# Optimization experiments

Hardware: AMD Instinct MI355X
Metric: run time of the kernel (lower is better)

The kernel has to match this reference:

```python
import itertools
import jax, jax.numpy as jnp
import numpy as np

THR = 0.2  # success_threshold (non-trainable constant)
V = 2      # num_total_variables
U_IDX, B_IDX = 1, 2  # rule_idxs for arities [0,1,2]


def _perm_indices(num_objects: int, v: int):
    """Static permutation index tables (numpy, shapes are compile-time)."""
    perm_idxs = np.array(list(itertools.permutations(range(num_objects), v)))  # [P, V]
    bidx = np.stack(np.nonzero(1 - np.eye(v))).T.reshape(v, v - 1, 2)          # [V, V-1, 2]
    pb = perm_idxs[:, bidx]                                                     # [P, V, V-1, 2]
    shift = (pb[..., 1] > pb[..., 0]).astype(np.int64)
    perm_bidxs = np.stack([pb[..., 0], pb[..., 1] - shift], axis=-1)            # off-diagonal compact idx
    return jnp.asarray(perm_idxs), jnp.asarray(perm_bidxs)


def setup_inputs() -> dict:
    key = jax.random.key(0)
    k1, k2, k3, k4, k5 = jax.random.split(key, 5)
    B, O, P0, P1, P2, C = 16, 64, 128, 128, 128, 8
    num_in = P0 + V * P1 + V * (V - 1) * P2  # 640
    return {
        "nullary": jax.random.normal(k1, (B, P0), dtype=jnp.float32),
        "unary": jax.random.normal(k2, (B, O, P1), dtype=jnp.float32),
        "binary": jax.random.normal(k3, (B, O, O - 1, P2), dtype=jnp.float32),
        "and_kernel": 0.01 * jax.random.normal(k4, (3, C, num_in), dtype=jnp.float32),
        "or_kernel": 0.01 * jax.random.normal(k5, (3, C), dtype=jnp.float32),
    }


def _forward(nullary, unary, binary, and_kernel, or_kernel):
    B, O, _ = unary.shape
    perm_idxs, perm_bidxs = _perm_indices(O, V)
    P = perm_idxs.shape[0]  # O*(O-1) for V=2
    thr = jnp.float32(THR)

    # permutation gathers -> flatten_concat with batch_dims=2
    pn = jnp.broadcast_to(nullary[:, None], (B, P, nullary.shape[-1]))          # [B,P,P0]
    pu = unary[:, perm_idxs].reshape(B, P, -1)                                   # [B,P,V*P1]
    pb = binary[:, perm_bidxs[..., 0], perm_bidxs[..., 1]].reshape(B, P, -1)     # [B,P,V*(V-1)*P2]
    x = jnp.concatenate([pn, pu, pb], axis=-1)                                   # [B,P,num_in]

    # AND stage: multiply-sum + bias + tanh (einsum == sum(in_tensor * and_kernel, -1))
    and_bias = thr - jnp.sum(jnp.square(and_kernel), -1) * jnp.tanh(thr)         # [A,C]
    conj = jnp.tanh(jnp.einsum('bpi,aci->bpac', x, and_kernel) + and_bias)       # [B,P,A,C]

    A, C = and_kernel.shape[0], and_kernel.shape[1]
    # OR max-reduce over unused permutation dims
    null_r = jnp.max(conj[:, :, :U_IDX, :], axis=1)                              # [B,n0,C]
    un_r = conj[:, :, U_IDX:B_IDX, :].reshape(B, O, P // O, B_IDX - U_IDX, C).max(axis=2)
    bi_r = conj[:, :, B_IDX:, :].reshape(B, O, O - 1, P // (O * (O - 1)), A - B_IDX, C).max(axis=3)

    def or_stage(c, k):
        bias = jnp.sum(jnp.square(k), -1) * jnp.tanh(thr) - thr                  # [n_rules]
        return jnp.einsum('...rc,rc->...r', c, k) + bias

    return (or_stage(null_r, or_kernel[:U_IDX]),
            or_stage(un_r, or_kernel[U_IDX:B_IDX]),
            or_stage(bi_r, or_kernel[B_IDX:]))


def reference(nullary, unary, binary, and_kernel, or_kernel):
    # outputs: nullary [B,1], unary [B,O,1], binary [B,O,O-1,1]
    return _forward(nullary, unary, binary, and_kernel, or_kernel)
```

## Files before the change

kernel.cpp:

```cpp
#include <hip/hip_runtime.h>

#define THR_F     0.2f
#define TANH_THR  0.19737532f

__device__ __forceinline__ float fast_tanh(float x) {
    x = fminf(10.f, fmaxf(-10.f, x));
    float e = __expf(2.f * x);
    return (e - 1.f) * __builtin_amdgcn_rcpf(e + 1.f);
}

__device__ __forceinline__ unsigned fkey(float f) {
    unsigned u = __float_as_uint(f);
    return (u & 0x80000000u) ? ~u : (u | 0x80000000u);
}
__device__ __forceinline__ float fdecode(unsigned u) {
    return __uint_as_float((u & 0x80000000u) ? (u & 0x7FFFFFFFu) : ~u);
}

__global__ __launch_bounds__(64) void prep_kernel(
    const float* __restrict__ nullary,
    const float* __restrict__ andk,
    float* __restrict__ Wb,
    float* __restrict__ Wu,
    float* __restrict__ base,
    unsigned* __restrict__ max0)
{
    const int bid = blockIdx.x;
    const int t   = threadIdx.x;
    if (bid < 384) {
        const int b = bid / 24, n = bid % 24;
        const float* w  = andk + n * 640;
        const float* nu = nullary + b * 128;
        float s = 0.f;
        #pragma unroll
        for (int i = 0; i < 10; ++i) { float v = w[t + i * 64]; s = fmaf(v, v, s); }
        float d = fmaf(nu[t], w[t], 0.f);
        d = fmaf(nu[t + 64], w[t + 64], d);
        #pragma unroll
        for (int m = 32; m; m >>= 1) {
            s += __shfl_xor(s, m, 64);
            d += __shfl_xor(d, m, 64);
        }
        if (t == 0) base[bid] = d + THR_F - s * TANH_THR;
    } else {
        const int i = (bid - 384) * 64 + t;
        const int k = i / 48, n = i % 48;
        const int ac   = (n < 24) ? n : n - 24;
        const int colb = (n < 24) ? 384 : 512;
        const int colu = (n < 24) ? 128 : 256;
        Wb[i] = andk[ac * 640 + colb + k];
        Wu[i] = andk[ac * 640 + colu + k];
        if (bid < 386) max0[(bid - 384) * 64 + t] = 0u;
    }
}

__global__ __launch_bounds__(256) void proj_kernel(
    const float* __restrict__ unary,
    const float* __restrict__ binary,
    const float* __restrict__ Wb,
    const float* __restrict__ Wu,
    float* __restrict__ P0,
    float* __restrict__ P1T,
    float* __restrict__ U0, float* __restrict__ U1)
{
    const int bid  = blockIdx.x;
    const int wave = __builtin_amdgcn_readfirstlane((int)(threadIdx.x >> 6));
    const int lane = threadIdx.x & 63;
    const bool is_bin = (bid < 1008);

    const int row = is_bin ? (bid * 64 + lane) : ((bid - 1008) * 64 + lane);
    const float* __restrict__ W   = (is_bin ? Wb : Wu) + wave * 12;
    const float* __restrict__ src = (is_bin ? binary : unary) + (size_t)row * 128;

    float* dst;
    if (is_bin) {
        if (wave < 2) {
            dst = P0 + (size_t)row * 24 + (wave & 1) * 12;
        } else {
            const int b   = row / 4032;
            const int rem = row - b * 4032;
            const int o   = rem / 63;
            const int j   = rem - o * 63;
            dst = P1T + ((size_t)(b * 63 + j) * 64 + o) * 24 + (wave & 1) * 12;
        }
    } else {
        dst = ((wave < 2) ? U0 : U1) + (size_t)row * 24 + (wave & 1) * 12;
    }

    float acc[12];
    #pragma unroll
    for (int n = 0; n < 12; ++n) acc[n] = 0.f;

    const float4* rp = (const float4*)src;
    #pragma unroll 8
    for (int k4 = 0; k4 < 32; ++k4) {
        float4 a = rp[k4];
        const float* wk = W + k4 * 4 * 48;
        #pragma unroll
        for (int q = 0; q < 4; ++q) {
            float av = (q == 0) ? a.x : (q == 1) ? a.y : (q == 2) ? a.z : a.w;
            const float* w = wk + q * 48;
            #pragma unroll
            for (int n = 0; n < 12; ++n) acc[n] = fmaf(av, w[n], acc[n]);
        }
    }

    float4* d4 = (float4*)dst;
    #pragma unroll
    for (int i = 0; i < 3; ++i)
        d4[i] = make_float4(acc[i*4+0], acc[i*4+1], acc[i*4+2], acc[i*4+3]);
}

__global__ __launch_bounds__(192) void combine_kernel(
    const float* __restrict__ base,
    const float* __restrict__ U0, const float* __restrict__ U1,
    const float* __restrict__ P0,
    const float* __restrict__ P1T,
    const float* __restrict__ ork,
    unsigned* __restrict__ max0,
    float* __restrict__ out)
{
    const int bid = blockIdx.x;
    const int b   = bid >> 6;
    const int o0  = bid & 63;
    const int a   = __builtin_amdgcn_readfirstlane((int)(threadIdx.x >> 6));
    const int t   = threadIdx.x & 63;
    const bool act = (t < 63);

    const int o1   = min(t + (t >= o0 ? 1 : 0), 63);
    const int jrow = min((t < o0) ? (o0 - 1) : o0, 62);
    const int j01  = min(t, 62);
    const int ch   = a * 8;

    const float* pb  = base + b * 24 + ch;
    const float* pa0 = U0 + (size_t)(b * 64 + o0) * 24 + ch;
    const float4* A1 = (const float4*)(U1 + (size_t)(b * 64 + o1) * 24 + ch);
    const float4* Q0 = (const float4*)(P0 + (size_t)((b * 64 + o0) * 63 + j01) * 24 + ch);
    const float4* Q1 = (const float4*)(P1T + ((size_t)(b * 63 + jrow) * 64 + o1) * 24 + ch);

    float th[8];
    #pragma unroll
    for (int i = 0; i < 2; ++i) {
        float4 a1 = A1[i], q0 = Q0[i], q1 = Q1[i];
        int n = i * 4;
        th[n+0] = pb[n+0] + pa0[n+0] + a1.x + q0.x + q1.x;
        th[n+1] = pb[n+1] + pa0[n+1] + a1.y + q0.y + q1.y;
        th[n+2] = pb[n+2] + pa0[n+2] + a1.z + q0.z + q1.z;
        th[n+3] = pb[n+3] + pa0[n+3] + a1.w + q0.w + q1.w;
    }
    #pragma unroll
    for (int n = 0; n < 8; ++n) th[n] = fast_tanh(th[n]);

    if (a == 2) {
        if (act) {
            float v = 0.f, b2 = 0.f;
            #pragma unroll
            for (int c = 0; c < 8; ++c) {
                float k = ork[16 + c];
                v  = fmaf(th[c], k, v);
                b2 = fmaf(k, k, b2);
            }
            out[16 + 1024 + ((b * 64 + o0) * 63 + t)] = v + b2 * TANH_THR - THR_F;
        }
        return;
    }

    if (!act) {
        #pragma unroll
        for (int n = 0; n < 8; ++n) th[n] = -2.0f;
    }
    #pragma unroll
    for (int n = 0; n < 8; ++n) {
        float v = th[n];
        #pragma unroll
        for (int m = 32; m; m >>= 1) v = fmaxf(v, __shfl_xor(v, m, 64));
        th[n] = v;
    }

    if (t == 0) {
        if (a == 1) {
            float v1 = 0.f, b1 = 0.f;
            #pragma unroll
            for (int c = 0; c < 8; ++c) {
                float k = ork[8 + c];
                v1 = fmaf(th[c], k, v1);
                b1 = fmaf(k, k, b1);
            }
            out[16 + b * 64 + o0] = v1 + b1 * TANH_THR - THR_F;
        } else {
            #pragma unroll
            for (int c = 0; c < 8; ++c)
                atomicMax(&max0[b * 8 + c], fkey(th[c]));
        }
    }
}

__global__ __launch_bounds__(64) void finalize_kernel(
    const unsigned* __restrict__ max0,
    const float* __restrict__ ork,
    float* __restrict__ out)
{
    int b = threadIdx.x;
    if (b >= 16) return;
    float v = 0.f, bb = 0.f;
    #pragma unroll
    for (int c = 0; c < 8; ++c) {
        float m = fdecode(max0[b * 8 + c]);
        float k = ork[c];
        v  = fmaf(m, k, v);
        bb = fmaf(k, k, bb);
    }
    out[b] = v + bb * TANH_THR - THR_F;
}

extern "C" void kernel_launch(void* const* d_in, const int* in_sizes, int n_in,
                              void* d_out, int out_size, void* d_ws, size_t ws_size,
                              hipStream_t stream)
{
    const float* nullary = (const float*)d_in[0];
    const float* unary   = (const float*)d_in[1];
    const float* binary  = (const float*)d_in[2];
    const float* andk    = (const float*)d_in[3];
    const float* ork     = (const float*)d_in[4];
    float* out = (float*)d_out;

    float* ws = (float*)d_ws;
    float*    base = ws;
    float*    U0   = ws + 384;
    float*    U1   = ws + 24960;
    float*    Wb   = ws + 49536;
    float*    Wu   = ws + 55680;
    float*    P0   = ws + 61824;
    float*    P1T  = ws + 1610112;
    unsigned* max0 = (unsigned*)(ws + 3158400);

    prep_kernel<<<480, 64, 0, stream>>>(nullary, andk, Wb, Wu, base, max0);
    proj_kernel<<<1024, 256, 0, stream>>>(unary, binary, Wb, Wu, P0, P1T, U0, U1);
    combine_kernel<<<1024, 192, 0, stream>>>(base, U0, U1, P0, P1T, ork, max0, out);
    finalize_kernel<<<1, 64, 0, stream>>>(max0, ork, out);
}
```

Before: 124.6 us.

## Store binary projections as bf16 and fold finalize into combine via last-block counter

The intermediate binary projections P0/P1T are now packed as bf16 pairs, halving their write traffic in proj_kernel and their read traffic in combine_kernel. The separate finalize kernel is removed. The last combine block, detected with an atomic counter after a threadfence, computes the nullary OR output instead. This trades bf16 rounding error on pre-tanh sums, plus an extra atomic per block, for less memory traffic and one fewer launch.

```diff
diff --git a/kernel.cpp b/kernel.cpp
--- a/kernel.cpp
+++ b/kernel.cpp
@@ -16,6 +16,16 @@
 __device__ __forceinline__ float fdecode(unsigned u) {
     return __uint_as_float((u & 0x80000000u) ? (u & 0x7FFFFFFFu) : ~u);
 }
+
+__device__ __forceinline__ unsigned pk_bf16(float lo, float hi) {
+    unsigned ul = __float_as_uint(lo);
+    unsigned uh = __float_as_uint(hi);
+    ul += 0x7FFFu + ((ul >> 16) & 1u);
+    uh += 0x7FFFu + ((uh >> 16) & 1u);
+    return (ul >> 16) | (uh & 0xFFFF0000u);
+}
+__device__ __forceinline__ float bf_lo(unsigned u) { return __uint_as_float(u << 16); }
+__device__ __forceinline__ float bf_hi(unsigned u) { return __uint_as_float(u & 0xFFFF0000u); }
 
 __global__ __launch_bounds__(64) void prep_kernel(
     const float* __restrict__ nullary,
@@ -50,7 +60,10 @@
         const int colu = (n < 24) ? 128 : 256;
         Wb[i] = andk[ac * 640 + colb + k];
         Wu[i] = andk[ac * 640 + colu + k];
-        if (bid < 386) max0[(bid - 384) * 64 + t] = 0u;
+        if (bid < 387) {
+            int idx = (bid - 384) * 64 + t;
+            if (idx < 192) max0[idx] = 0u;
+        }
     }
 }
 
@@ -59,8 +72,8 @@
     const float* __restrict__ binary,
     const float* __restrict__ Wb,
     const float* __restrict__ Wu,
-    float* __restrict__ P0,
-    float* __restrict__ P1T,
+    unsigned* __restrict__ P0,
+    unsigned* __restrict__ P1T,
     float* __restrict__ U0, float* __restrict__ U1)
 {
     const int bid  = blockIdx.x;
@@ -72,50 +85,56 @@
     const float* __restrict__ W   = (is_bin ? Wb : Wu) + wave * 12;
     const float* __restrict__ src = (is_bin ? binary : unary) + (size_t)row * 128;
 
-    float* dst;
+    float acc[12];
+    #pragma unroll
+    for (int n = 0; n < 12; ++n) acc[n] = 0.f;
+
+    const float4* rp = (const float4*)src;
+    #pragma unroll 8
+    for (int k4 = 0; k4 < 32; ++k4) {
+        float4 a = rp[k4];
+        const float* wk = W + k4 * 4 * 48;
+        #pragma unroll
+        for (int q = 0; q < 4; ++q) {
+            float av = (q == 0) ? a.x : (q == 1) ? a.y : (q == 2) ? a.z : a.w;
+            const float* w = wk + q * 48;
+            #pragma unroll
+            for (int n = 0; n < 12; ++n) acc[n] = fmaf(av, w[n], acc[n]);
+        }
+    }
+
     if (is_bin) {
+        unsigned* dstp;
         if (wave < 2) {
-            dst = P0 + (size_t)row * 24 + (wave & 1) * 12;
+            dstp = P0 + (size_t)row * 12 + (wave & 1) * 6;
         } else {
             const int b   = row / 4032;
             const int rem = row - b * 4032;
             const int o   = rem / 63;
             const int j   = rem - o * 63;
-            dst = P1T + ((size_t)(b * 63 + j) * 64 + o) * 24 + (wave & 1) * 12;
-        }
+            dstp = P1T + ((size_t)(b * 63 + j) * 64 + o) * 12 + (wave & 1) * 6;
+        }
+        unsigned pk[6];
+        #pragma unroll
+        for (int i = 0; i < 6; ++i) pk[i] = pk_bf16(acc[2*i], acc[2*i+1]);
+        uint2* d2 = (uint2*)dstp;
+        d2[0] = make_uint2(pk[0], pk[1]);
+        d2[1] = make_uint2(pk[2], pk[3]);
+        d2[2] = make_uint2(pk[4], pk[5]);
     } else {
-        dst = ((wave < 2) ? U0 : U1) + (size_t)row * 24 + (wave & 1) * 12;
-    }
-
-    float acc[12];
-    #pragma unroll
-    for (int n = 0; n < 12; ++n) acc[n] = 0.f;
-
-    const float4* rp = (const float4*)src;
-    #pragma unroll 8
-    for (int k4 = 0; k4 < 32; ++k4) {
-        float4 a = rp[k4];
-        const float* wk = W + k4 * 4 * 48;
-        #pragma unroll
-        for (int q = 0; q < 4; ++q) {
-            float av = (q == 0) ? a.x : (q == 1) ? a.y : (q == 2) ? a.z : a.w;
-            const float* w = wk + q * 48;
-            #pragma unroll
-            for (int n = 0; n < 12; ++n) acc[n] = fmaf(av, w[n], acc[n]);
-        }
-    }
-
-    float4* d4 = (float4*)dst;
-    #pragma unroll
-    for (int i = 0; i < 3; ++i)
-        d4[i] = make_float4(acc[i*4+0], acc[i*4+1], acc[i*4+2], acc[i*4+3]);
+        float* dst = ((wave < 2) ? U0 : U1) + (size_t)row * 24 + (wave & 1) * 12;
+        float4* d4 = (float4*)dst;
+        #pragma unroll
+        for (int i = 0; i < 3; ++i)
+            d4[i] = make_float4(acc[i*4+0], acc[i*4+1], acc[i*4+2], acc[i*4+3]);
+    }
 }
 
 __global__ __launch_bounds__(192) void combine_kernel(
     const float* __restrict__ base,
     const float* __restrict__ U0, const float* __restrict__ U1,
-    const float* __restrict__ P0,
-    const float* __restrict__ P1T,
+    const unsigned* __restrict__ P0,
+    const unsigned* __restrict__ P1T,
     const float* __restrict__ ork,
     unsigned* __restrict__ max0,
     float* __restrict__ out)
@@ -135,19 +154,21 @@
     const float* pb  = base + b * 24 + ch;
     const float* pa0 = U0 + (size_t)(b * 64 + o0) * 24 + ch;
     const float4* A1 = (const float4*)(U1 + (size_t)(b * 64 + o1) * 24 + ch);
-    const float4* Q0 = (const float4*)(P0 + (size_t)((b * 64 + o0) * 63 + j01) * 24 + ch);
-    const float4* Q1 = (const float4*)(P1T + ((size_t)(b * 63 + jrow) * 64 + o1) * 24 + ch);
+    const uint4*  Q0 = (const uint4*)(P0 + (size_t)((b * 64 + o0) * 63 + j01) * 12 + a * 4);
+    const uint4*  Q1 = (const uint4*)(P1T + ((size_t)(b * 63 + jrow) * 64 + o1) * 12 + a * 4);
+
+    uint4 q0 = *Q0, q1 = *Q1;
+    float4 a1l = A1[0], a1h = A1[1];
 
     float th[8];
-    #pragma unroll
-    for (int i = 0; i < 2; ++i) {
-        float4 a1 = A1[i], q0 = Q0[i], q1 = Q1[i];
-        int n = i * 4;
-        th[n+0] = pb[n+0] + pa0[n+0] + a1.x + q0.x + q1.x;
-        th[n+1] = pb[n+1] + pa0[n+1] + a1.y + q0.y + q1.y;
-        th[n+2] = pb[n+2] + pa0[n+2] + a1.z + q0.z + q1.z;
-        th[n+3] = pb[n+3] + pa0[n+3] + a1.w + q0.w + q1.w;
-    }
+    th[0] = pb[0] + pa0[0] + a1l.x + bf_lo(q0.x) + bf_lo(q1.x);
+    th[1] = pb[1] + pa0[1] + a1l.y + bf_hi(q0.x) + bf_hi(q1.x);
+    th[2] = pb[2] + pa0[2] + a1l.z + bf_lo(q0.y) + bf_lo(q1.y);
+    th[3] = pb[3] + pa0[3] + a1l.w + bf_hi(q0.y) + bf_hi(q1.y);
+    th[4] = pb[4] + pa0[4] + a1h.x + bf_lo(q0.z) + bf_lo(q1.z);
+    th[5] = pb[5] + pa0[5] + a1h.y + bf_hi(q0.z) + bf_hi(q1.z);
+    th[6] = pb[6] + pa0[6] + a1h.z + bf_lo(q0.w) + bf_lo(q1.w);
+    th[7] = pb[7] + pa0[7] + a1h.w + bf_hi(q0.w) + bf_hi(q1.w);
     #pragma unroll
     for (int n = 0; n < 8; ++n) th[n] = fast_tanh(th[n]);
 
@@ -177,8 +198,8 @@
         th[n] = v;
     }
 
-    if (t == 0) {
-        if (a == 1) {
+    if (a == 1) {
+        if (t == 0) {
             float v1 = 0.f, b1 = 0.f;
             #pragma unroll
             for (int c = 0; c < 8; ++c) {
@@ -187,30 +208,30 @@
                 b1 = fmaf(k, k, b1);
             }
             out[16 + b * 64 + o0] = v1 + b1 * TANH_THR - THR_F;
-        } else {
-            #pragma unroll
-            for (int c = 0; c < 8; ++c)
-                atomicMax(&max0[b * 8 + c], fkey(th[c]));
-        }
-    }
-}
-
-__global__ __launch_bounds__(64) void finalize_kernel(
-    const unsigned* __restrict__ max0,
-    const float* __restrict__ ork,
-    float* __restrict__ out)
-{
-    int b = threadIdx.x;
-    if (b >= 16) return;
-    float v = 0.f, bb = 0.f;
-    #pragma unroll
-    for (int c = 0; c < 8; ++c) {
-        float m = fdecode(max0[b * 8 + c]);
-        float k = ork[c];
-        v  = fmaf(m, k, v);
-        bb = fmaf(k, k, bb);
-    }
-    out[b] = v + bb * TANH_THR - THR_F;
+        }
+        return;
+    }
+
+    unsigned rank = 0u;
+    if (t == 0) {
+        #pragma unroll
+        for (int c = 0; c < 8; ++c)
+            atomicMax(&max0[b * 8 + c], fkey(th[c]));
+        __threadfence();
+        rank = atomicAdd(&max0[128], 1u) + 1u;
+    }
+    rank = __shfl(rank, 0, 64);
+    if (rank == 1024u && t < 16) {
+        float v = 0.f, bb = 0.f;
+        #pragma unroll
+        for (int c = 0; c < 8; ++c) {
+            float m = fdecode(atomicAdd(&max0[t * 8 + c], 0u));
+            float k = ork[c];
+            v  = fmaf(m, k, v);
+            bb = fmaf(k, k, bb);
+        }
+        out[t] = v + bb * TANH_THR - THR_F;
+    }
 }
 
 extern "C" void kernel_launch(void* const* d_in, const int* in_sizes, int n_in,
@@ -230,12 +251,11 @@
     float*    U1   = ws + 24960;
     float*    Wb   = ws + 49536;
     float*    Wu   = ws + 55680;
-    float*    P0   = ws + 61824;
-    float*    P1T  = ws + 1610112;
-    unsigned* max0 = (unsigned*)(ws + 3158400);
+    unsigned* P0   = (unsigned*)(ws + 61824);
+    unsigned* P1T  = (unsigned*)(ws + 835968);
+    unsigned* max0 = (unsigned*)(ws + 1610112);
 
     prep_kernel<<<480, 64, 0, stream>>>(nullary, andk, Wb, Wu, base, max0);
     proj_kernel<<<1024, 256, 0, stream>>>(unary, binary, Wb, Wu, P0, P1T, U0, U1);
     combine_kernel<<<1024, 192, 0, stream>>>(base, U0, U1, P0, P1T, ork, max0, out);
-    finalize_kernel<<<1, 64, 0, stream>>>(max0, ork, out);
-}
+}
```

Measured after the change: 138.9 us. 11.5% more time.
